# Performance work log

Measured on AMD Instinct MI355X. Metric: run time of the kernel, lower is better.

## Reference

```python
import jax, jax.numpy as jnp
import numpy as np

SR_S = 4  # search_range_spatial
SR_D = 2  # search_range_depth


def setup_inputs() -> dict:
    key = jax.random.key(0)
    k1, k2, k3, k4 = jax.random.split(key, 4)
    b, c, h, w, d = 1, 32, 80, 80, 20
    return {
        'mpi1_features': jax.random.normal(k1, (b, c, h, w, d), jnp.float32),
        'mpi1_alpha': jax.random.uniform(k3, (b, 1, h, w, d), jnp.float32),
        'mpi2_features': jax.random.normal(k2, (b, c, h, w, d), jnp.float32),
        'mpi2_alpha': jax.random.uniform(k4, (b, 1, h, w, d), jnp.float32),
    }


def _correlation(mpi1_features, mpi1_alpha, mpi2_features, mpi2_alpha):
    so = 2 * SR_S + 1  # spatial_output_dim = 9
    do = 2 * SR_D + 1  # depth_output_dim = 5
    b, c, h, w, d = mpi1_features.shape
    ca = mpi1_alpha.shape[1]
    # visibility masks: any alpha along depth -> clip to [0,1], broadcast over depth
    mask1 = jnp.clip(jnp.sum(mpi1_alpha, axis=-1, keepdims=True), 0.0, 1.0)
    mask2 = jnp.clip(jnp.sum(mpi2_alpha, axis=-1, keepdims=True), 0.0, 1.0)
    mask1 = jnp.broadcast_to(mask1, mpi1_alpha.shape)
    mask2 = jnp.broadcast_to(mask2, mpi1_alpha.shape)
    pad = ((0, 0), (0, 0), (SR_S, SR_S), (SR_S, SR_S), (SR_D, SR_D))
    f2p = jnp.pad(mpi2_features, pad)                      # zeros, like F.pad default
    m2p = jnp.pad(mask2, pad, constant_values=1.0)         # mask padded with 1
    # displacement grid in torch loop order: k (depth) outer, then i, then j
    kk, ii, jj = jnp.meshgrid(jnp.arange(do), jnp.arange(so), jnp.arange(so), indexing='ij')
    disp = jnp.stack([ii.ravel(), jj.ravel(), kk.ravel()], axis=1)  # [D, 3]

    def step(carry, ijk):
        i, j, k = ijk[0], ijk[1], ijk[2]
        f2s = jax.lax.dynamic_slice(f2p, (0, 0, i, j, k), (b, c, h, w, d))
        m2s = jax.lax.dynamic_slice(m2p, (0, 0, i, j, k), (b, ca, h, w, d))
        cost = jnp.mean(mpi1_features * f2s, axis=1)                 # [b,h,w,d]
        cm = jnp.clip(jnp.sum(mask1 * m2s, axis=1), 0.0, 1.0)        # [b,h,w,d]
        return carry, (cost, cm)

    _, (cv, cvm) = jax.lax.scan(step, None, disp)
    # [D,b,h,w,d] -> [b,D,h,w,d]  (D = do*so*so = 405 channels, torch cat order)
    cost_volume = jnp.moveaxis(cv, 0, 1)
    cost_volume_mask = jnp.moveaxis(cvm, 0, 1)
    return cost_volume, cost_volume_mask


def reference(mpi1_features, mpi1_alpha, mpi2_features, mpi2_alpha):
    return _correlation(mpi1_features, mpi1_alpha, mpi2_features, mpi2_alpha)
```

## Files before the change

kernel.cpp:

```cpp
#include <hip/hip_runtime.h>

#define H 80
#define W 80
#define DD 20
#define C 32
#define NPOS (H*W)
#define NP3 (NPOS*DD)
#define SO 9
#define DO_ 5
#define NDISP (DO_*SO*SO)

#define NC 8
#define NCHUNK (C/NC)
#define XQ 20
#define COLS 28
#define ZST 28
#define CHUNK_FLOATS (NC*COLS*ZST)

typedef float nt4 __attribute__((ext_vector_type(4)));

__global__ __launch_bounds__(320, 4)
void fused_kernel(const float* __restrict__ f1, const float* __restrict__ a1,
                  const float* __restrict__ f2, const float* __restrict__ a2,
                  float* __restrict__ outc, float* __restrict__ outm)
{
    __shared__ __align__(16) float f2s[2][CHUNK_FLOATS];
    __shared__ float m1s[XQ];
    __shared__ float m2s[COLS];

    int bid = blockIdx.x;
    int swz = (bid & 7) * 360 + (bid >> 3);
    int y  = swz / 36;
    int r0 = swz % 36;
    int di = r0 >> 2;
    int xq = r0 & 3;

    int t   = threadIdx.x;
    int djg = t / 100;
    int r   = t % 100;
    int xl  = r / 5;
    int zg  = r % 5;
    int z0  = zg * 4;
    int x   = xq * XQ + xl;
    int pos = y * W + x;
    int y2  = y + di - 4;
    bool y2ok = ((unsigned)y2 < (unsigned)H);
    bool act  = (t < 300);

    int s    = t - 96;
    int sc_  = s / COLS;
    int scol = s % COLS;
    int sx2  = xq * XQ + scol - 4;
    bool stager = (t >= 96) && y2ok && ((unsigned)sx2 < (unsigned)W);
    const float* sp_base = stager ? (f2 + (size_t)sc_ * NP3 + (y2 * W + sx2) * DD) : f2;
    float* sd = &f2s[0][0] + (sc_ * COLS + scol) * ZST + 2;

    for (int i = t; i < 2 * CHUNK_FLOATS / 4; i += 320)
        ((float4*)f2s)[i] = make_float4(0.f, 0.f, 0.f, 0.f);

    if (t < XQ){
        const float* p = a1 + (y * W + xq * XQ + t) * DD;
        float sm = 0.f;
        #pragma unroll
        for (int q = 0; q < 5; ++q){
            float4 v = *(const float4*)(p + q * 4);
            sm += v.x + v.y + v.z + v.w;
        }
        m1s[t] = fminf(fmaxf(sm, 0.f), 1.f);
    } else if (t >= 32 && t < 32 + COLS){
        int col = t - 32;
        int x2 = xq * XQ + col - 4;
        float m = 1.f;
        if (y2ok && ((unsigned)x2 < (unsigned)W)){
            const float* p = a2 + (y2 * W + x2) * DD;
            float sm = 0.f;
            #pragma unroll
            for (int q = 0; q < 5; ++q){
                float4 v = *(const float4*)(p + q * 4);
                sm += v.x + v.y + v.z + v.w;
            }
            m = fminf(fmaxf(sm, 0.f), 1.f);
        }
        m2s[col] = m;
    }
    __syncthreads();

    if (stager){
        #pragma unroll
        for (int q = 0; q < 5; ++q){
            float4 v = *(const float4*)(sp_base + q * 4);
            *(float2*)(sd + q * 4)     = make_float2(v.x, v.y);
            *(float2*)(sd + q * 4 + 2) = make_float2(v.z, v.w);
        }
    }
    __syncthreads();

    float acc[3][DO_][4];
    #pragma unroll
    for (int i = 0; i < 3; ++i)
        #pragma unroll
        for (int j = 0; j < DO_; ++j)
            #pragma unroll
            for (int k = 0; k < 4; ++k) acc[i][j][k] = 0.f;

    const float* a_base = f1 + pos * DD + z0;

    #pragma unroll 1
    for (int cc = 0; cc < NCHUNK; ++cc){
        if (cc < NCHUNK - 1 && stager){
            const float* p = sp_base + (size_t)(cc + 1) * NC * NP3;
            float* d = sd + ((cc + 1) & 1) * CHUNK_FLOATS;
            #pragma unroll
            for (int q = 0; q < 5; ++q){
                float4 v = *(const float4*)(p + q * 4);
                *(float2*)(d + q * 4)     = make_float2(v.x, v.y);
                *(float2*)(d + q * 4 + 2) = make_float2(v.z, v.w);
            }
        }
        if (act){
            const float* base = &f2s[cc & 1][0];
            #pragma unroll
            for (int c = 0; c < NC; ++c){
                float4 avv = *(const float4*)(a_base + (size_t)(cc * NC + c) * NP3);
                float av[4] = {avv.x, avv.y, avv.z, avv.w};
                #pragma unroll
                for (int djl = 0; djl < 3; ++djl){
                    int dj = djg * 3 + djl;
                    const float* bp = base + (c * COLS + xl + dj) * ZST + z0;
                    float4 b0 = *(const float4*)(bp);
                    float4 b1 = *(const float4*)(bp + 4);
                    float bb[8] = {b0.x, b0.y, b0.z, b0.w, b1.x, b1.y, b1.z, b1.w};
                    #pragma unroll
                    for (int dk = 0; dk < DO_; ++dk)
                        #pragma unroll
                        for (int z = 0; z < 4; ++z)
                            acc[djl][dk][z] = fmaf(av[z], bb[z + dk], acc[djl][dk][z]);
                }
            }
        }
        if (cc < NCHUNK - 1) __syncthreads();
    }

    if (act){
        const float sc = 1.0f / 32.0f;
        float m1v = m1s[xl];
        #pragma unroll
        for (int djl = 0; djl < 3; ++djl){
            int dj = djg * 3 + djl;
            float m2v = m2s[xl + dj];
            float mi = fminf(m1v * m2v, 1.f);
            #pragma unroll
            for (int dk = 0; dk < DO_; ++dk){
                size_t off = (size_t)(dk * 81 + di * 9 + dj) * NP3 + pos * DD + z0;
                nt4 wv;
                wv.x = acc[djl][dk][0] * sc;
                wv.y = acc[djl][dk][1] * sc;
                wv.z = acc[djl][dk][2] * sc;
                wv.w = acc[djl][dk][3] * sc;
                __builtin_nontemporal_store(wv, (nt4*)(outc + off));
                int zlo = 2 - dk, zhi = 22 - dk;
                nt4 mv;
                mv.x = (z0 + 0 >= zlo && z0 + 0 < zhi) ? mi : m1v;
                mv.y = (z0 + 1 >= zlo && z0 + 1 < zhi) ? mi : m1v;
                mv.z = (z0 + 2 >= zlo && z0 + 2 < zhi) ? mi : m1v;
                mv.w = (z0 + 3 >= zlo && z0 + 3 < zhi) ? mi : m1v;
                __builtin_nontemporal_store(mv, (nt4*)(outm + off));
            }
        }
    }
}

extern "C" void kernel_launch(void* const* d_in, const int* in_sizes, int n_in,
                              void* d_out, int out_size, void* d_ws, size_t ws_size,
                              hipStream_t stream)
{
    const float* f1 = (const float*)d_in[0];
    const float* a1 = (const float*)d_in[1];
    const float* f2 = (const float*)d_in[2];
    const float* a2 = (const float*)d_in[3];
    float* outc = (float*)d_out;
    float* outm = outc + (size_t)NDISP * NP3;
    (void)d_ws; (void)ws_size; (void)in_sizes; (void)n_in;

    fused_kernel<<<80 * SO * 4, 320, 0, stream>>>(f1, a1, f2, a2, outc, outm);
}
```

Before: 576.7 us.

## Halve channel chunk, prefetch next chunk into registers, use plain output stores

Drops the channels per staged chunk from 8 to 4, which halves the shared-memory double buffer and doubles the number of chunk iterations. The next chunk's global loads now go into registers before the compute and are written to shared memory afterwards, so load latency overlaps the FMA work. Staging moves to threads 0..111, which also compute. The launch-bounds minimum-occupancy hint is removed, and nontemporal output stores become ordinary float4 stores. These changes trade register pressure and extra barriers against better overlap, and the store change may affect cache behaviour on the large output writes.

New measurement: 557.9 us. 1.03x faster.

```diff
diff --git a/kernel.cpp b/kernel.cpp
--- a/kernel.cpp
+++ b/kernel.cpp
@@ -10,16 +10,14 @@
 #define DO_ 5
 #define NDISP (DO_*SO*SO)
 
-#define NC 8
+#define NC 4
 #define NCHUNK (C/NC)
 #define XQ 20
 #define COLS 28
 #define ZST 28
 #define CHUNK_FLOATS (NC*COLS*ZST)
 
-typedef float nt4 __attribute__((ext_vector_type(4)));
-
-__global__ __launch_bounds__(320, 4)
+__global__ __launch_bounds__(320)
 void fused_kernel(const float* __restrict__ f1, const float* __restrict__ a1,
                   const float* __restrict__ f2, const float* __restrict__ a2,
                   float* __restrict__ outc, float* __restrict__ outm)
@@ -47,13 +45,12 @@
     bool y2ok = ((unsigned)y2 < (unsigned)H);
     bool act  = (t < 300);
 
-    int s    = t - 96;
-    int sc_  = s / COLS;
-    int scol = s % COLS;
+    int sc_  = t / COLS;
+    int scol = t % COLS;
     int sx2  = xq * XQ + scol - 4;
-    bool stager = (t >= 96) && y2ok && ((unsigned)sx2 < (unsigned)W);
+    bool stager = (t < NC * COLS) && y2ok && ((unsigned)sx2 < (unsigned)W);
     const float* sp_base = stager ? (f2 + (size_t)sc_ * NP3 + (y2 * W + sx2) * DD) : f2;
-    float* sd = &f2s[0][0] + (sc_ * COLS + scol) * ZST + 2;
+    float* sd0 = &f2s[0][0] + (sc_ * COLS + scol) * ZST + 2;
 
     for (int i = t; i < 2 * CHUNK_FLOATS / 4; i += 320)
         ((float4*)f2s)[i] = make_float4(0.f, 0.f, 0.f, 0.f);
@@ -89,8 +86,8 @@
         #pragma unroll
         for (int q = 0; q < 5; ++q){
             float4 v = *(const float4*)(sp_base + q * 4);
-            *(float2*)(sd + q * 4)     = make_float2(v.x, v.y);
-            *(float2*)(sd + q * 4 + 2) = make_float2(v.z, v.w);
+            *(float2*)(sd0 + q * 4)     = make_float2(v.x, v.y);
+            *(float2*)(sd0 + q * 4 + 2) = make_float2(v.z, v.w);
         }
     }
     __syncthreads();
@@ -107,15 +104,12 @@
 
     #pragma unroll 1
     for (int cc = 0; cc < NCHUNK; ++cc){
-        if (cc < NCHUNK - 1 && stager){
+        bool doStage = (cc < NCHUNK - 1) && stager;
+        float4 st[5];
+        if (doStage){
             const float* p = sp_base + (size_t)(cc + 1) * NC * NP3;
-            float* d = sd + ((cc + 1) & 1) * CHUNK_FLOATS;
             #pragma unroll
-            for (int q = 0; q < 5; ++q){
-                float4 v = *(const float4*)(p + q * 4);
-                *(float2*)(d + q * 4)     = make_float2(v.x, v.y);
-                *(float2*)(d + q * 4 + 2) = make_float2(v.z, v.w);
-            }
+            for (int q = 0; q < 5; ++q) st[q] = *(const float4*)(p + q * 4);
         }
         if (act){
             const float* base = &f2s[cc & 1][0];
@@ -138,6 +132,14 @@
                 }
             }
         }
+        if (doStage){
+            float* d = sd0 + ((cc + 1) & 1) * CHUNK_FLOATS;
+            #pragma unroll
+            for (int q = 0; q < 5; ++q){
+                *(float2*)(d + q * 4)     = make_float2(st[q].x, st[q].y);
+                *(float2*)(d + q * 4 + 2) = make_float2(st[q].z, st[q].w);
+            }
+        }
         if (cc < NCHUNK - 1) __syncthreads();
     }
 
@@ -152,19 +154,19 @@
             #pragma unroll
             for (int dk = 0; dk < DO_; ++dk){
                 size_t off = (size_t)(dk * 81 + di * 9 + dj) * NP3 + pos * DD + z0;
-                nt4 wv;
+                float4 wv;
                 wv.x = acc[djl][dk][0] * sc;
                 wv.y = acc[djl][dk][1] * sc;
                 wv.z = acc[djl][dk][2] * sc;
                 wv.w = acc[djl][dk][3] * sc;
-                __builtin_nontemporal_store(wv, (nt4*)(outc + off));
+                *(float4*)(outc + off) = wv;
                 int zlo = 2 - dk, zhi = 22 - dk;
-                nt4 mv;
+                float4 mv;
                 mv.x = (z0 + 0 >= zlo && z0 + 0 < zhi) ? mi : m1v;
                 mv.y = (z0 + 1 >= zlo && z0 + 1 < zhi) ? mi : m1v;
                 mv.z = (z0 + 2 >= zlo && z0 + 2 < zhi) ? mi : m1v;
                 mv.w = (z0 + 3 >= zlo && z0 + 3 < zhi) ? mi : m1v;
-                __builtin_nontemporal_store(mv, (nt4*)(outm + off));
+                *(float4*)(outm + off) = mv;
             }
         }
     }
```

## Replace double-buffered f2 staging with single buffer to cut LDS use

Applied to the files above, without the earlier changes.

Drops the two-slot LDS ping-pong for the f2 chunk in favor of one buffer, staged and consumed each iteration between two barriers. Also prefetches f1 channel values in groups of four before the barrier and removes the minimum-blocks launch bound. The intent is to halve LDS per block and ease register pressure so more blocks fit per CU. The cost is that global loads for the next chunk no longer overlap compute, and each chunk now needs an extra barrier.

Result: slower. 592.1 us (+2.7%).

```diff
diff --git a/kernel.cpp b/kernel.cpp
--- a/kernel.cpp
+++ b/kernel.cpp
@@ -15,16 +15,16 @@
 #define XQ 20
 #define COLS 28
 #define ZST 28
-#define CHUNK_FLOATS (NC*COLS*ZST)
+#define F2S_FLOATS (NC*COLS*ZST)
 
 typedef float nt4 __attribute__((ext_vector_type(4)));
 
-__global__ __launch_bounds__(320, 4)
+__global__ __launch_bounds__(320)
 void fused_kernel(const float* __restrict__ f1, const float* __restrict__ a1,
                   const float* __restrict__ f2, const float* __restrict__ a2,
                   float* __restrict__ outc, float* __restrict__ outm)
 {
-    __shared__ __align__(16) float f2s[2][CHUNK_FLOATS];
+    __shared__ __align__(16) float f2s[F2S_FLOATS];
     __shared__ float m1s[XQ];
     __shared__ float m2s[COLS];
 
@@ -48,14 +48,14 @@
     bool act  = (t < 300);
 
     int s    = t - 96;
-    int sc_  = s / COLS;
+    int sc8  = s / COLS;
     int scol = s % COLS;
     int sx2  = xq * XQ + scol - 4;
     bool stager = (t >= 96) && y2ok && ((unsigned)sx2 < (unsigned)W);
-    const float* sp_base = stager ? (f2 + (size_t)sc_ * NP3 + (y2 * W + sx2) * DD) : f2;
-    float* sd = &f2s[0][0] + (sc_ * COLS + scol) * ZST + 2;
+    const float* sp_base = stager ? (f2 + (size_t)sc8 * NP3 + (y2 * W + sx2) * DD) : f2;
+    float* sd = f2s + (sc8 * COLS + scol) * ZST + 2;
 
-    for (int i = t; i < 2 * CHUNK_FLOATS / 4; i += 320)
+    for (int i = t; i < F2S_FLOATS / 4; i += 320)
         ((float4*)f2s)[i] = make_float4(0.f, 0.f, 0.f, 0.f);
 
     if (t < XQ){
@@ -85,16 +85,6 @@
     }
     __syncthreads();
 
-    if (stager){
-        #pragma unroll
-        for (int q = 0; q < 5; ++q){
-            float4 v = *(const float4*)(sp_base + q * 4);
-            *(float2*)(sd + q * 4)     = make_float2(v.x, v.y);
-            *(float2*)(sd + q * 4 + 2) = make_float2(v.z, v.w);
-        }
-    }
-    __syncthreads();
-
     float acc[3][DO_][4];
     #pragma unroll
     for (int i = 0; i < 3; ++i)
@@ -107,38 +97,54 @@
 
     #pragma unroll 1
     for (int cc = 0; cc < NCHUNK; ++cc){
-        if (cc < NCHUNK - 1 && stager){
-            const float* p = sp_base + (size_t)(cc + 1) * NC * NP3;
-            float* d = sd + ((cc + 1) & 1) * CHUNK_FLOATS;
+        if (stager){
+            const float* p = sp_base + (size_t)cc * NC * NP3;
             #pragma unroll
             for (int q = 0; q < 5; ++q){
                 float4 v = *(const float4*)(p + q * 4);
-                *(float2*)(d + q * 4)     = make_float2(v.x, v.y);
-                *(float2*)(d + q * 4 + 2) = make_float2(v.z, v.w);
+                *(float2*)(sd + q * 4)     = make_float2(v.x, v.y);
+                *(float2*)(sd + q * 4 + 2) = make_float2(v.z, v.w);
             }
         }
+        float av[4][4];
         if (act){
-            const float* base = &f2s[cc & 1][0];
             #pragma unroll
-            for (int c = 0; c < NC; ++c){
-                float4 avv = *(const float4*)(a_base + (size_t)(cc * NC + c) * NP3);
-                float av[4] = {avv.x, avv.y, avv.z, avv.w};
+            for (int c = 0; c < 4; ++c){
+                float4 v = *(const float4*)(a_base + (size_t)(cc * NC + c) * NP3);
+                av[c][0] = v.x; av[c][1] = v.y; av[c][2] = v.z; av[c][3] = v.w;
+            }
+        }
+        __syncthreads();
+        if (act){
+            #pragma unroll
+            for (int half = 0; half < 2; ++half){
+                if (half == 1){
+                    #pragma unroll
+                    for (int c = 0; c < 4; ++c){
+                        float4 v = *(const float4*)(a_base + (size_t)(cc * NC + 4 + c) * NP3);
+                        av[c][0] = v.x; av[c][1] = v.y; av[c][2] = v.z; av[c][3] = v.w;
+                    }
+                }
                 #pragma unroll
-                for (int djl = 0; djl < 3; ++djl){
-                    int dj = djg * 3 + djl;
-                    const float* bp = base + (c * COLS + xl + dj) * ZST + z0;
-                    float4 b0 = *(const float4*)(bp);
-                    float4 b1 = *(const float4*)(bp + 4);
-                    float bb[8] = {b0.x, b0.y, b0.z, b0.w, b1.x, b1.y, b1.z, b1.w};
+                for (int c = 0; c < 4; ++c){
+                    int c8 = half * 4 + c;
                     #pragma unroll
-                    for (int dk = 0; dk < DO_; ++dk)
+                    for (int djl = 0; djl < 3; ++djl){
+                        int dj = djg * 3 + djl;
+                        const float* bp = f2s + (c8 * COLS + xl + dj) * ZST + z0;
+                        float4 b0 = *(const float4*)(bp);
+                        float4 b1 = *(const float4*)(bp + 4);
+                        float bb[8] = {b0.x, b0.y, b0.z, b0.w, b1.x, b1.y, b1.z, b1.w};
                         #pragma unroll
-                        for (int z = 0; z < 4; ++z)
-                            acc[djl][dk][z] = fmaf(av[z], bb[z + dk], acc[djl][dk][z]);
+                        for (int dk = 0; dk < DO_; ++dk)
+                            #pragma unroll
+                            for (int z = 0; z < 4; ++z)
+                                acc[djl][dk][z] = fmaf(av[c][z], bb[z + dk], acc[djl][dk][z]);
+                    }
                 }
             }
         }
-        if (cc < NCHUNK - 1) __syncthreads();
+        __syncthreads();
     }
 
     if (act){
```
